# Optimization experiments

Hardware: AMD Instinct MI355X
Metric: run time of the kernel (lower is better)

The kernel has to match this reference:

```python
import jax, jax.numpy as jnp
import numpy as np

N, BS, T, D = 512, 64, 200, 32
ALPHA, EPS, TIME_LOG, POWER = 0.1, 1e-6, 5.0, 3


def setup_inputs() -> dict:
    key = jax.random.key(0)
    ks = jax.random.split(key, 16)
    s = 0.1
    skills = jax.random.randint(ks[0], (BS, T), 0, N)
    times = jnp.sort(jax.random.randint(ks[1], (BS, T), 0, 100000), axis=1)
    labels = jax.random.uniform(ks[2], (BS, T), dtype=jnp.float32)
    adj = jax.random.uniform(ks[3], (1, BS, N, N), dtype=jnp.float32)
    node_embeddings = jax.random.normal(ks[4], (1, N, 2 * D), dtype=jnp.float32)
    user_b0 = jax.random.uniform(ks[5], (BS, D), dtype=jnp.float32)
    user_f0 = jax.random.uniform(ks[6], (BS, D), dtype=jnp.float32)
    conv1_w = jax.random.normal(ks[7], (D, D, 5), dtype=jnp.float32) * s
    conv1_b = jax.random.normal(ks[8], (D,), dtype=jnp.float32) * s
    conv2_w = jax.random.normal(ks[9], (D, D, 1), dtype=jnp.float32) * s
    conv2_b = jax.random.normal(ks[10], (D,), dtype=jnp.float32) * s
    lin_f_w = jax.random.normal(ks[11], (D, D), dtype=jnp.float32) * s
    lin_f_b = jax.random.normal(ks[12], (D,), dtype=jnp.float32) * s
    lin_b_w = jax.random.normal(ks[13], (D, D), dtype=jnp.float32) * s
    lin_b_b = jax.random.normal(ks[14], (D,), dtype=jnp.float32) * s
    return dict(skills=skills, times=times, labels=labels, adj=adj,
                node_embeddings=node_embeddings, user_b0=user_b0, user_f0=user_f0,
                conv1_w=conv1_w, conv1_b=conv1_b, conv2_w=conv2_w, conv2_b=conv2_b,
                lin_f_w=lin_f_w, lin_f_b=lin_f_b, lin_b_w=lin_b_w, lin_b_b=lin_b_b)


def _forward(skills, times, labels, adj, node_embeddings, user_b0, user_f0,
             conv1_w, conv1_b, conv2_w, conv2_b, lin_f_w, lin_f_b, lin_b_w, lin_b_b):
    n = jnp.float32(N)
    A1 = adj[0]                      # [BS, N, N]  (leading A=1 dim squeezed)
    A2 = jnp.matmul(A1, A1)
    A3 = jnp.matmul(A2, A1)
    # adj^i / N^i for i=1..3, stacked over power dim -> [BS, 3, N, N]
    adj_list = jnp.stack([A1 / n, A2 / (n * n), A3 / (n * n * n)], axis=1)
    node_emb = node_embeddings[0]    # [N, 2D]
    node_send, node_rec = node_emb[:, :D], node_emb[:, D:]
    # temporal deltas: log(|t_i - t_{i-1}| + EPS) / log(time_log) -> [T-1, BS]
    dt = jnp.abs(times[:, 1:] - times[:, :-1]).astype(jnp.float32)
    delta = (jnp.log(dt + EPS) / jnp.log(jnp.float32(TIME_LOG))).T

    last_perf0 = user_b0 @ node_rec.T           # [BS, N]
    node_last_forget0 = user_f0 @ node_send.T   # [BS, N]

    def step(carry, xs):
        user_b, user_f, last_perf, node_last_forget = carry
        delta_t, label_t, skill_t = xs
        node_cur_base = user_b @ node_rec.T                               # [BS, N]
        temporal = jnp.exp(-delta_t[:, None] * ALPHA * node_last_forget) * last_perf
        # sum over powers folded into the contraction; /(power*N) as in source
        spatial = jnp.einsum('bj,bnjk->bk', last_perf, adj_list) / (POWER * n)
        cur_perf = jax.nn.sigmoid(node_cur_base + temporal + spatial)     # [BS, N]
        nlf = user_f @ node_send.T
        lab = jnp.broadcast_to(label_t[:, None], (BS, D))
        user = jnp.stack([user_b, user_f, lab,
                          node_rec[skill_t], node_send[skill_t]], axis=-1)  # [BS, D, 5]
        h = jax.nn.relu(jnp.einsum('bcl,ocl->bo', user, conv1_w) + conv1_b)
        uu = h @ conv2_w[:, :, 0].T + conv2_b
        new_f = jnp.tanh(uu @ lin_f_w.T + lin_f_b)
        new_b = jnp.tanh(uu @ lin_b_w.T + lin_b_b)
        pred = jnp.take_along_axis(cur_perf, skill_t[:, None], axis=1)    # [BS, 1]
        return (new_b, new_f, cur_perf, nlf), pred

    xs = (delta, labels[:, 1:].T, skills[:, 1:].T)
    _, preds = jax.lax.scan(step, (user_b0, user_f0, last_perf0, node_last_forget0), xs)
    return preds  # [T-1, BS, 1]


def reference(skills, times, labels, adj, node_embeddings, user_b0, user_f0,
              conv1_w, conv1_b, conv2_w, conv2_b, lin_f_w, lin_f_b, lin_b_w, lin_b_b):
    return _forward(skills, times, labels, adj, node_embeddings, user_b0, user_f0,
                    conv1_w, conv1_b, conv2_w, conv2_b, lin_f_w, lin_f_b, lin_b_w, lin_b_b)
```

## Files before the change

kernel.cpp:

```cpp
#include <hip/hip_runtime.h>

#define NN 512
#define BSZ 64
#define TTOT 200
#define NSTEP 199
#define DD 32

typedef __attribute__((ext_vector_type(8))) short bf16x8;
typedef __attribute__((ext_vector_type(8))) int i32x8;
typedef __attribute__((ext_vector_type(4))) float f32x4;
typedef __attribute__((ext_vector_type(4))) unsigned int u32x4;

__device__ __forceinline__ float bf2f(unsigned short u) {
  union { unsigned int i; float f; } v; v.i = ((unsigned int)u) << 16; return v.f;
}
__device__ __forceinline__ unsigned short f2bf(float f) {
  unsigned int b = __float_as_uint(f);
  return (unsigned short)((b + 0x7fffu + ((b >> 16) & 1u)) >> 16);
}
__device__ __forceinline__ unsigned int pk_trunc(float hi, float lo) {
  return __builtin_amdgcn_perm(__float_as_uint(hi), __float_as_uint(lo), 0x07060302u);
}
__device__ __forceinline__ unsigned char e4m3(float x) {
  float a = fabsf(x);
  unsigned int s = (__float_as_uint(x) >> 24) & 0x80u;
  if (a < 0.01171875f) return (unsigned char)s;
  a = fminf(a, 448.0f);
  unsigned int u = __float_as_uint(a);
  unsigned int keep = (u >> 20) & 7u;
  unsigned int rest = u & 0xFFFFFu;
  unsigned int base = (((u >> 23) - 120u) << 3) | keep;
  unsigned int rnd = (rest > 0x80000u) || (rest == 0x80000u && (keep & 1u));
  return (unsigned char)(s | (base + rnd));
}
__device__ __forceinline__ float dec8(unsigned char x) {
  int e = (x >> 3) & 15, m = x & 7;
  float v = e ? ldexpf(8.f + (float)m, e - 10) : ldexpf((float)m, -9);
  return (x & 0x80) ? -v : v;
}
__device__ __forceinline__ float rlane(float v, int l) {
  return __int_as_float(__builtin_amdgcn_readlane(__float_as_int(v), l));
}

__device__ __forceinline__ size_t m8_addr(int k, int col) {
  int nt = col >> 4, cch = k >> 5;
  int l2 = (((k >> 3) & 3) << 4) + (col & 15);
  return (size_t)((nt * 16 + cch) * 512) + (size_t)l2 * 8 + (size_t)(k & 7);
}
__device__ __forceinline__ size_t m8mxa(int k, int col) {
  int f = ((k >> 7) << 5) + (col >> 4);
  int ln2 = (((k >> 5) & 3) << 4) + (col & 15);
  return (((size_t)f * 64 + ln2) << 5) + (size_t)(k & 31);
}

__global__ __launch_bounds__(256) void gemm_a2_fast(
    const float* __restrict__ A1, unsigned short* __restrict__ A2) {
  const int tn = blockIdx.x, tm = blockIdx.y, b = blockIdx.z;
  const int tid = threadIdx.x, lane = tid & 63;
  const int w = tid >> 6, wr = w >> 1, wc = w & 1;
  const int q = lane >> 4, ln = lane & 15;
  const size_t Ao = (size_t)b * NN * NN;
  __shared__ __align__(16) unsigned char Asw[128 * 128];
  __shared__ __align__(16) unsigned char Bsw[128 * 128];
  f32x4 acc[4][4];
#pragma unroll
  for (int mi = 0; mi < 4; ++mi)
#pragma unroll
    for (int ni = 0; ni < 4; ++ni) acc[mi][ni] = f32x4{0.f, 0.f, 0.f, 0.f};

  const int arow = tid >> 2, achk = tid & 3;
  const int bg = tid >> 5, bc0 = (tid & 31) * 4;
  const float* Ab = A1 + Ao;

  for (int k0 = 0; k0 < NN; k0 += 64) {
#pragma unroll
    for (int p = 0; p < 2; ++p) {
      const int r = arow + p * 64;
      const float* src = Ab + (size_t)(tm * 128 + r) * NN + k0 + achk * 16;
      f32x4 x0 = *(const f32x4*)src, x1 = *(const f32x4*)(src + 4);
      f32x4 x2 = *(const f32x4*)(src + 8), x3 = *(const f32x4*)(src + 12);
      u32x4 y0 = u32x4{pk_trunc(x0[1], x0[0]), pk_trunc(x0[3], x0[2]),
                       pk_trunc(x1[1], x1[0]), pk_trunc(x1[3], x1[2])};
      u32x4 y1 = u32x4{pk_trunc(x2[1], x2[0]), pk_trunc(x2[3], x2[2]),
                       pk_trunc(x3[1], x3[0]), pk_trunc(x3[3], x3[2])};
      const int sw = r & 7;
      *(u32x4*)(Asw + r * 128 + (((achk * 2) ^ sw) << 4)) = y0;
      *(u32x4*)(Asw + r * 128 + (((achk * 2 + 1) ^ sw) << 4)) = y1;
    }
    {
      f32x4 r[8];
#pragma unroll
      for (int i = 0; i < 8; ++i)
        r[i] = *(const f32x4*)(Ab + (size_t)(k0 + bg * 8 + i) * NN + tn * 128 + bc0);
#pragma unroll
      for (int m = 0; m < 4; ++m) {
        const int col = bc0 + m;
        u32x4 v = u32x4{pk_trunc(r[1][m], r[0][m]), pk_trunc(r[3][m], r[2][m]),
                        pk_trunc(r[5][m], r[4][m]), pk_trunc(r[7][m], r[6][m])};
        *(u32x4*)(Bsw + col * 128 + ((bg ^ (col & 7)) << 4)) = v;
      }
    }
    __syncthreads();
#pragma unroll
    for (int ks = 0; ks < 2; ++ks) {
      bf16x8 af[4], bv[4];
#pragma unroll
      for (int mi = 0; mi < 4; ++mi) {
        const int r = wr * 64 + mi * 16 + ln;
        af[mi] = *(const bf16x8*)(Asw + r * 128 + (((ks * 4 + q) ^ (r & 7)) << 4));
      }
#pragma unroll
      for (int ni = 0; ni < 4; ++ni) {
        const int r = wc * 64 + ni * 16 + ln;
        bv[ni] = *(const bf16x8*)(Bsw + r * 128 + (((ks * 4 + q) ^ (r & 7)) << 4));
      }
#pragma unroll
      for (int mi = 0; mi < 4; ++mi)
#pragma unroll
        for (int ni = 0; ni < 4; ++ni)
          acc[mi][ni] = __builtin_amdgcn_mfma_f32_16x16x32_bf16(
              af[mi], bv[ni], acc[mi][ni], 0, 0, 0);
    }
    __syncthreads();
  }
  unsigned short* Cb = A2 + Ao;
#pragma unroll
  for (int mi = 0; mi < 4; ++mi)
#pragma unroll
    for (int ni = 0; ni < 4; ++ni) {
      const int col = tn * 128 + wc * 64 + ni * 16 + ln;
#pragma unroll
      for (int r = 0; r < 4; ++r) {
        const int row = tm * 128 + wr * 64 + mi * 16 + q * 4 + r;
        Cb[(size_t)row * NN + col] = f2bf(acc[mi][ni][r]);
      }
    }
}

__global__ __launch_bounds__(256) void gemm_m_fast(
    const float* __restrict__ A1, const unsigned short* __restrict__ A2,
    unsigned char* __restrict__ M8k, unsigned char* __restrict__ M8x,
    int has_mx) {
  const int tn = blockIdx.x, tm = blockIdx.y, b = blockIdx.z;
  const int tid = threadIdx.x, lane = tid & 63;
  const int w = tid >> 6, wr = w >> 1, wc = w & 1;
  const int q = lane >> 4, ln = lane & 15;
  const size_t Ao = (size_t)b * NN * NN;
  __shared__ __align__(16) unsigned char Asw[128 * 128];
  __shared__ __align__(16) unsigned char Bsw[128 * 128];
  f32x4 acc[4][4];
#pragma unroll
  for (int mi = 0; mi < 4; ++mi)
#pragma unroll
    for (int ni = 0; ni < 4; ++ni) acc[mi][ni] = f32x4{0.f, 0.f, 0.f, 0.f};

  const int srow = tid >> 1, sh = tid & 1;
  const int bg = tid >> 5, bc0 = (tid & 31) * 4;
  const unsigned short* A2b = A2 + Ao;
  const float* Ab = A1 + Ao;

  for (int k0 = 0; k0 < NN; k0 += 64) {
    {
      const unsigned short* asrc = A2b + (size_t)(tm * 128 + srow) * NN + k0 + sh * 32;
      const int sw = srow & 7;
#pragma unroll
      for (int j = 0; j < 4; ++j) {
        u32x4 va = *(const u32x4*)(asrc + j * 8);
        *(u32x4*)(Asw + srow * 128 + (((sh * 4 + j) ^ sw) << 4)) = va;
      }
    }
    {
      f32x4 r[8];
#pragma unroll
      for (int i = 0; i < 8; ++i)
        r[i] = *(const f32x4*)(Ab + (size_t)(k0 + bg * 8 + i) * NN + tn * 128 + bc0);
#pragma unroll
      for (int m = 0; m < 4; ++m) {
        const int col = bc0 + m;
        u32x4 v = u32x4{pk_trunc(r[1][m], r[0][m]), pk_trunc(r[3][m], r[2][m]),
                        pk_trunc(r[5][m], r[4][m]), pk_trunc(r[7][m], r[6][m])};
        *(u32x4*)(Bsw + col * 128 + ((bg ^ (col & 7)) << 4)) = v;
      }
    }
    __syncthreads();
#pragma unroll
    for (int ks = 0; ks < 2; ++ks) {
      bf16x8 af[4], bv[4];
#pragma unroll
      for (int mi = 0; mi < 4; ++mi) {
        const int r = wr * 64 + mi * 16 + ln;
        af[mi] = *(const bf16x8*)(Asw + r * 128 + (((ks * 4 + q) ^ (r & 7)) << 4));
      }
#pragma unroll
      for (int ni = 0; ni < 4; ++ni) {
        const int r = wc * 64 + ni * 16 + ln;
        bv[ni] = *(const bf16x8*)(Bsw + r * 128 + (((ks * 4 + q) ^ (r & 7)) << 4));
      }
#pragma unroll
      for (int mi = 0; mi < 4; ++mi)
#pragma unroll
        for (int ni = 0; ni < 4; ++ni)
          acc[mi][ni] = __builtin_amdgcn_mfma_f32_16x16x32_bf16(
              af[mi], bv[ni], acc[mi][ni], 0, 0, 0);
    }
    __syncthreads();
  }
  const float c1 = 1048576.f / (3.f * 512.f * 512.f);
  const float c2 = c1 / 512.f;
  const float c3 = c2 / 512.f;
  unsigned char* Mk = M8k + Ao;
  unsigned char* Mx = M8x + Ao;
#pragma unroll
  for (int mi = 0; mi < 4; ++mi) {
    const int row0 = tm * 128 + wr * 64 + mi * 16 + q * 4;
#pragma unroll
    for (int ni = 0; ni < 4; ++ni) {
      const int col = tn * 128 + wc * 64 + ni * 16 + ln;
      unsigned int wv = 0;
#pragma unroll
      for (int r = 0; r < 4; ++r) {
        const int row = row0 + r;
        float mval = c1 * A1[Ao + (size_t)row * NN + col] +
                     c2 * bf2f(A2b[(size_t)row * NN + col]) + c3 * acc[mi][ni][r];
        wv |= ((unsigned int)e4m3(mval)) << (8 * r);
      }
      *(unsigned int*)(Mk + m8_addr(row0, col)) = wv;
      if (has_mx) *(unsigned int*)(Mx + m8mxa(row0, col)) = wv;
    }
  }
}

__global__ __launch_bounds__(256) void gemm_a2_slow(
    const float* __restrict__ A1, unsigned short* __restrict__ A2) {
  const int b = blockIdx.x, tn = blockIdx.y, tm = blockIdx.z;
  const int tid = threadIdx.x, lane = tid & 63, w = tid >> 6;
  const int q = lane >> 4, ln = lane & 15;
  const size_t Ao = (size_t)b * NN * NN;
  f32x4 zero = {0.f, 0.f, 0.f, 0.f};
  f32x4 acc[4] = {zero, zero, zero, zero};
  const float* ap = A1 + Ao + (size_t)(tm * 64 + w * 16 + ln) * NN + q * 8;
  for (int k0 = 0; k0 < NN; k0 += 32) {
    f32x4 x0 = *(const f32x4*)(ap + k0);
    f32x4 x1 = *(const f32x4*)(ap + k0 + 4);
    union { bf16x8 v; unsigned int u[4]; } af;
    af.u[0] = pk_trunc(x0[1], x0[0]);
    af.u[1] = pk_trunc(x0[3], x0[2]);
    af.u[2] = pk_trunc(x1[1], x1[0]);
    af.u[3] = pk_trunc(x1[3], x1[2]);
#pragma unroll
    for (int i = 0; i < 4; ++i) {
      bf16x8 bv;
#pragma unroll
      for (int j = 0; j < 8; ++j)
        bv[j] = (short)f2bf(A1[Ao + (size_t)(k0 + q * 8 + j) * NN + tn * 64 + i * 16 + ln]);
      acc[i] = __builtin_amdgcn_mfma_f32_16x16x32_bf16(af.v, bv, acc[i], 0, 0, 0);
    }
  }
  unsigned short* Cb = A2 + Ao;
#pragma unroll
  for (int i = 0; i < 4; ++i) {
    int col = tn * 64 + i * 16 + ln;
#pragma unroll
    for (int r = 0; r < 4; ++r) {
      int row = tm * 64 + w * 16 + q * 4 + r;
      Cb[(size_t)row * NN + col] = f2bf(acc[i][r]);
    }
  }
}

__global__ __launch_bounds__(256) void gemm_m_slow(
    const float* __restrict__ A1, const unsigned short* __restrict__ A2,
    unsigned char* __restrict__ M8k, unsigned char* __restrict__ M8x,
    int has_mx) {
  const int b = blockIdx.x, tn = blockIdx.y, tm = blockIdx.z;
  const int tid = threadIdx.x, lane = tid & 63, w = tid >> 6;
  const int q = lane >> 4, ln = lane & 15;
  const size_t Ao = (size_t)b * NN * NN;
  const unsigned short* A2b = A2 + Ao;
  f32x4 zero = {0.f, 0.f, 0.f, 0.f};
  f32x4 acc[4] = {zero, zero, zero, zero};
  const unsigned short* ap = A2b + (size_t)(tm * 64 + w * 16 + ln) * NN + q * 8;
  for (int k0 = 0; k0 < NN; k0 += 32) {
    bf16x8 af = *(const bf16x8*)(ap + k0);
#pragma unroll
    for (int i = 0; i < 4; ++i) {
      bf16x8 bv;
#pragma unroll
      for (int j = 0; j < 8; ++j)
        bv[j] = (short)f2bf(A1[Ao + (size_t)(k0 + q * 8 + j) * NN + tn * 64 + i * 16 + ln]);
      acc[i] = __builtin_amdgcn_mfma_f32_16x16x32_bf16(af, bv, acc[i], 0, 0, 0);
    }
  }
  const float c1 = 1048576.f / (3.f * 512.f * 512.f);
  const float c2 = c1 / 512.f;
  const float c3 = c2 / 512.f;
  unsigned char* Mk = M8k + Ao;
  unsigned char* Mx = M8x + Ao;
  const int row0 = tm * 64 + w * 16 + q * 4;
#pragma unroll
  for (int i = 0; i < 4; ++i) {
    int col = tn * 64 + i * 16 + ln;
    unsigned int wv = 0;
#pragma unroll
    for (int r = 0; r < 4; ++r) {
      int row = row0 + r;
      float mval = c1 * A1[Ao + (size_t)row * NN + col] +
                   c2 * bf2f(A2b[(size_t)row * NN + col]) + c3 * acc[i][r];
      wv |= ((unsigned int)e4m3(mval)) << (8 * r);
    }
    *(unsigned int*)(Mk + m8_addr(row0, col)) = wv;
    if (has_mx) *(unsigned int*)(Mx + m8mxa(row0, col)) = wv;
  }
}

__global__ __launch_bounds__(64) void probe_kernel(int* __restrict__ flag) {
  const int lane = threadIdx.x, q = lane >> 4, n = lane & 15;
  __shared__ unsigned char A8[128];
  __shared__ unsigned char B8[128 * 16];
  for (int k = lane; k < 128; k += 64) A8[k] = (unsigned char)(8 + ((k * 37 + 11) % 56));
  for (int i = lane; i < 2048; i += 64)
    B8[i] = (unsigned char)(((i & 1) ? 0x80 : 0) | (8 + ((i * 23 + 5) % 56)));
  __syncthreads();
  union { i32x8 v; unsigned char b[32]; } af, bf;
#pragma unroll
  for (int j = 0; j < 32; ++j) {
    af.b[j] = A8[q * 32 + j];
    bf.b[j] = B8[(q * 32 + j) * 16 + n];
  }
  f32x4 acc = {0.f, 0.f, 0.f, 0.f};
  acc = __builtin_amdgcn_mfma_scale_f32_16x16x128_f8f6f4(af.v, bf.v, acc, 0, 0,
                                                         0, 127, 0, 127);
  float ref = 0.f;
  for (int k = 0; k < 128; ++k) ref += dec8(A8[k]) * dec8(B8[k * 16 + n]);
  int ok = 1;
#pragma unroll
  for (int r = 0; r < 4; ++r)
    ok &= (fabsf(acc[r] - ref) <= 1e-3f * fmaxf(fabsf(ref), 1.f)) ? 1 : 0;
  unsigned long long bal = __ballot(ok);
  if (lane == 0) *flag = (bal == ~0ull) ? 1 : 0;
}

__global__ __launch_bounds__(64) void traj2_kernel(
    const int* __restrict__ skills, const float* __restrict__ labels,
    const float* __restrict__ emb, const float* __restrict__ ub0g,
    const float* __restrict__ uf0g, const float* __restrict__ w1g,
    const float* __restrict__ b1g, const float* __restrict__ w2g,
    const float* __restrict__ b2g, const float* __restrict__ wfg,
    const float* __restrict__ bfg, const float* __restrict__ wbg,
    const float* __restrict__ bbg, float* __restrict__ UBg,
    float* __restrict__ UFg) {
  const int b = blockIdx.x;
  const int lane = threadIdx.x;
  const int o = lane & 31, half = lane >> 5;

  __shared__ float ub_l[DD], uf_l[DD], e_l[2 * DD];
  __shared__ float label_s[NSTEP];
  __shared__ int skill_s[NSTEP];

  for (int i = lane; i < NSTEP; i += 64) {
    label_s[i] = labels[b * TTOT + i + 1];
    skill_s[i] = skills[b * TTOT + i + 1];
  }

  float w1r[80];
#pragma unroll
  for (int k = 0; k < 8; ++k) {
    const int c0 = (half * 8 + k) * 2;
#pragma unroll
    for (int j = 0; j < 5; ++j) {
      w1r[k * 10 + j] = w1g[o * 160 + c0 * 5 + j];
      w1r[k * 10 + 5 + j] = w1g[o * 160 + (c0 + 1) * 5 + j];
    }
  }
  float w2r[16];
#pragma unroll
  for (int cc = 0; cc < 16; ++cc) w2r[cc] = w2g[o * 32 + half * 16 + cc];
  const float* wsg = half ? wbg : wfg;
  float wsr[32];
#pragma unroll
  for (int c = 0; c < DD; ++c) wsr[c] = wsg[o * 32 + c];
  const float b1r = b1g[o], b2r = b2g[o];
  const float bselr = half ? bbg[o] : bfg[o];

  float val = half ? ub0g[b * DD + o] : uf0g[b * DD + o];

  __syncthreads();

  float* UBp = UBg + (size_t)b * NSTEP * DD;
  float* UFp = UFg + (size_t)b * NSTEP * DD;

  float ev = emb[(size_t)skill_s[0] * (2 * DD) + lane];
  float pg[8];

  for (int step = 0; step < NSTEP; ++step) {
    if (step) {
      float part = 0.f;
#pragma unroll
      for (int s2 = 0; s2 < 8; ++s2) part += pg[s2];
      float h = b1r + part + __shfl_xor(part, 32);
      h = fmaxf(h, 0.f);
      float up = 0.f;
#pragma unroll
      for (int cc = 0; cc < 16; ++cc) {
        float hv0 = rlane(h, cc), hv1 = rlane(h, 16 + cc);
        up += (half ? hv1 : hv0) * w2r[cc];
      }
      float uu = b2r + up + __shfl_xor(up, 32);
      float aac = bselr;
#pragma unroll
      for (int c = 0; c < DD; ++c) aac += rlane(uu, c) * wsr[c];
      val = 1.f - 2.f / (1.f + __expf(2.f * aac));
    }
    if (half) ub_l[o] = val; else uf_l[o] = val;
    e_l[lane] = ev;
    (half ? UBp : UFp)[step * DD + o] = val;
    if (step + 1 < NSTEP) ev = emb[(size_t)skill_s[step + 1] * (2 * DD) + lane];
    const float lab = label_s[step];
#pragma unroll
    for (int k = 0; k < 8; ++k) {
      const int c0 = (half * 8 + k) * 2;
      float ubc0 = ub_l[c0], ubc1 = ub_l[c0 + 1];
      float ufc0 = uf_l[c0], ufc1 = uf_l[c0 + 1];
      float rs0 = e_l[c0], rs1 = e_l[c0 + 1];
      float rr0 = e_l[DD + c0], rr1 = e_l[DD + c0 + 1];
      float hpart = ubc0 * w1r[k * 10 + 0] + ufc0 * w1r[k * 10 + 1] +
                    lab * w1r[k * 10 + 2] + rr0 * w1r[k * 10 + 3] +
                    rs0 * w1r[k * 10 + 4];
      hpart += ubc1 * w1r[k * 10 + 5] + ufc1 * w1r[k * 10 + 6] +
               lab * w1r[k * 10 + 7] + rr1 * w1r[k * 10 + 8] +
               rs1 * w1r[k * 10 + 9];
      pg[k] = hpart;
    }
  }
}

__global__ __launch_bounds__(512) void precomp_kernel(
    const int* __restrict__ times, const float* __restrict__ emb,
    const float* __restrict__ UBg, const float* __restrict__ UFg,
    float* __restrict__ NCBg, float* __restrict__ TCg) {
  const int b = blockIdx.x;
  const int s0 = blockIdx.y * 8;
  const int n = threadIdx.x;
  float nr[DD], ns[DD];
#pragma unroll
  for (int c = 0; c < DD; ++c) {
    ns[c] = emb[(size_t)n * (2 * DD) + c];
    nr[c] = emb[(size_t)n * (2 * DD) + DD + c];
  }
  for (int s = s0; s < s0 + 8 && s < NSTEP; ++s) {
    const float* ubp = UBg + ((size_t)b * NSTEP + s) * DD;
    const float* ufp = UFg + ((size_t)b * NSTEP + (s ? s - 1 : 0)) * DD;
    float n0 = 0.f, n1 = 0.f, n2 = 0.f, n3 = 0.f;
    float l0 = 0.f, l1 = 0.f, l2 = 0.f, l3 = 0.f;
#pragma unroll
    for (int c = 0; c < 8; ++c) {
      n0 += ubp[c] * nr[c];
      n1 += ubp[8 + c] * nr[8 + c];
      n2 += ubp[16 + c] * nr[16 + c];
      n3 += ubp[24 + c] * nr[24 + c];
      l0 += ufp[c] * ns[c];
      l1 += ufp[8 + c] * ns[8 + c];
      l2 += ufp[16 + c] * ns[16 + c];
      l3 += ufp[24 + c] * ns[24 + c];
    }
    float ncb = (n0 + n1) + (n2 + n3);
    float nlf = (l0 + l1) + (l2 + l3);
    int dt_ = times[b * TTOT + s + 1] - times[b * TTOT + s];
    if (dt_ < 0) dt_ = -dt_;
    float delta = __logf((float)dt_ + 1e-6f) * 0.6213349345596119f;
    float tc = __expf(-delta * 0.1f * nlf);
    NCBg[((size_t)b * NSTEP + s) * NN + n] = ncb;
    TCg[((size_t)b * NSTEP + s) * NN + n] = tc;
  }
}

__global__ __launch_bounds__(512, 1) void scan_fast(
    const int* __restrict__ skills, const float* __restrict__ NCBg,
    const float* __restrict__ TCg, const unsigned char* __restrict__ M8k,
    const unsigned char* __restrict__ M8x, int allow_mx,
    const int* __restrict__ flag, float* __restrict__ out) {
  const int b = blockIdx.x;
  const int t = threadIdx.x;
  const int lane = t & 63, w = t >> 6, q = lane >> 4;
  __shared__ __align__(32) unsigned char lp8[2][NN];
  __shared__ int skill_s[NSTEP];
  const int use_mx = allow_mx && (*flag);
  for (int i = t; i < NSTEP; i += 512) skill_s[i] = skills[b * TTOT + i + 1];

  union MU { i32x8 v; long l[4]; };
  MU mreg[16];
  if (use_mx) {
    const unsigned char* Mb = M8x + (size_t)b * NN * NN;
#pragma unroll
    for (int c = 0; c < 4; ++c)
#pragma unroll
      for (int i = 0; i < 4; ++i)
        mreg[c * 4 + i].v = *(const i32x8*)(
            Mb + (((size_t)(c * 32 + w * 4 + i) * 64 + lane) << 5));
  } else {
    const unsigned char* Mb = M8k + (size_t)b * NN * NN;
#pragma unroll
    for (int c = 0; c < 16; ++c)
#pragma unroll
      for (int i = 0; i < 4; ++i)
        mreg[c].l[i] = *(const long*)(
            Mb + (((size_t)(w * 64 + i * 16 + c)) << 9) + (size_t)lane * 8);
  }
  const float* ncbp = NCBg + (size_t)b * NSTEP * NN + t;
  const float* tcp = TCg + (size_t)b * NSTEP * NN + t;
  float ncb_c = ncbp[0];
  float tc_c = tcp[0];
  float ncb_n1 = 0.f, tc_n1 = 1.f;
  if (NSTEP > 1) { ncb_n1 = ncbp[NN]; tc_n1 = tcp[NN]; }
  float rlp = ncb_c;
  lp8[0][t] = e4m3(rlp);
  __syncthreads();

  int pidx = -1;
  float pval = 0.f;
  for (int step = 0; step < NSTEP; ++step) {
    const int cb = step & 1;
    if (pidx >= 0) out[pidx] = pval;
    float ncb_n2 = 0.f, tc_n2 = 1.f;
    if (step + 2 < NSTEP) {
      ncb_n2 = ncbp[(size_t)(step + 2) * NN];
      tc_n2 = tcp[(size_t)(step + 2) * NN];
    }
    int sk_s = skill_s[step];
    f32x4 zero = {0.f, 0.f, 0.f, 0.f};
    f32x4 acc[4] = {zero, zero, zero, zero};
    if (use_mx) {
#pragma unroll
      for (int c = 0; c < 4; ++c) {
        i32x8 af = *(const i32x8*)(&lp8[cb][c * 128 + q * 32]);
#pragma unroll
        for (int i = 0; i < 4; ++i)
          acc[i] = __builtin_amdgcn_mfma_scale_f32_16x16x128_f8f6f4(
              af, mreg[c * 4 + i].v, acc[i], 0, 0, 0, 127, 0, 127);
      }
    } else {
#pragma unroll
      for (int c = 0; c < 16; ++c) {
        long af = *(const long*)(&lp8[cb][c * 32 + q * 8]);
#pragma unroll
        for (int i = 0; i < 4; ++i)
          acc[i] = __builtin_amdgcn_mfma_f32_16x16x32_fp8_fp8(af, mreg[c].l[i],
                                                              acc[i], 0, 0, 0);
      }
    }
    float spatial = ((q & 2) ? ((q & 1) ? acc[3][0] : acc[2][0])
                             : ((q & 1) ? acc[1][0] : acc[0][0])) * 0x1p-20f;
    float cur = 1.f / (1.f + __expf(-((ncb_c + tc_c * rlp) + spatial)));
    pidx = (t == sk_s) ? (step * BSZ + b) : -1;
    pval = cur;
    rlp = cur;
    lp8[cb ^ 1][t] = e4m3(cur);
    __syncthreads();
    ncb_c = ncb_n1; tc_c = tc_n1;
    ncb_n1 = ncb_n2; tc_n1 = tc_n2;
  }
  if (pidx >= 0) out[pidx] = pval;
}

__global__ __launch_bounds__(512, 2) void scan_kernel(
    const int* __restrict__ skills, const int* __restrict__ times,
    const float* __restrict__ labels, const float* __restrict__ emb,
    const float* __restrict__ ub0g, const float* __restrict__ uf0g,
    const float* __restrict__ w1g, const float* __restrict__ b1g,
    const float* __restrict__ w2g, const float* __restrict__ b2g,
    const float* __restrict__ wfg, const float* __restrict__ bfg,
    const float* __restrict__ wbg, const float* __restrict__ bbg,
    const unsigned char* __restrict__ M8k, const unsigned char* __restrict__ M8x,
    int allow_mx, const int* __restrict__ flag, float* __restrict__ out) {
  const int b = blockIdx.x;
  const int t = threadIdx.x;
  const int lane = t & 63, w = t >> 6, q = lane >> 4;

  __shared__ __align__(32) unsigned char lp8[NN];
  __shared__ float ub[DD], uf[DD];
  __shared__ float delta_s[NSTEP], label_s[NSTEP];
  __shared__ int skill_s[NSTEP];
  __shared__ float hp[16][33];
  __shared__ float w1t[DD * 5 * DD];
  __shared__ float w2t[DD * DD], wft[DD * DD], wbt[DD * DD];
  __shared__ float b1s[DD], b2s[DD], bfs[DD], bbs[DD];

  const int use_mx = allow_mx && (*flag);

  float nrec[DD], nsend[DD];
#pragma unroll
  for (int c = 0; c < DD; ++c) {
    nsend[c] = emb[(size_t)t * (2 * DD) + c];
    nrec[c] = emb[(size_t)t * (2 * DD) + DD + c];
  }
  for (int idx = t; idx < DD * DD * 5; idx += 512) {
    int o = idx / 160, rem = idx % 160;
    w1t[rem * 32 + o] = w1g[idx];
  }
  for (int idx = t; idx < DD * DD; idx += 512) {
    int o = idx >> 5, c = idx & 31;
    w2t[c * 32 + o] = w2g[idx];
    wft[c * 32 + o] = wfg[idx];
    wbt[c * 32 + o] = wbg[idx];
  }
  if (t < DD) {
    b1s[t] = b1g[t]; b2s[t] = b2g[t];
    bfs[t] = bfg[t]; bbs[t] = bbg[t];
    ub[t] = ub0g[b * DD + t];
    uf[t] = uf0g[b * DD + t];
  }
  for (int i = t; i < NSTEP; i += 512) {
    int dt_ = times[b * TTOT + i + 1] - times[b * TTOT + i];
    if (dt_ < 0) dt_ = -dt_;
    delta_s[i] = __logf((float)dt_ + 1e-6f) * 0.6213349345596119f;
    label_s[i] = labels[b * TTOT + i + 1];
    skill_s[i] = skills[b * TTOT + i + 1];
  }

  union MU { i32x8 v; long l[4]; };
  MU mreg[16];
  if (use_mx) {
    const unsigned char* Mb = M8x + (size_t)b * NN * NN;
#pragma unroll
    for (int c = 0; c < 4; ++c)
#pragma unroll
      for (int i = 0; i < 4; ++i)
        mreg[c * 4 + i].v = *(const i32x8*)(
            Mb + (((size_t)(c * 32 + w * 4 + i) * 64 + lane) << 5));
  } else {
    const unsigned char* Mb = M8k + (size_t)b * NN * NN;
#pragma unroll
    for (int c = 0; c < 16; ++c)
#pragma unroll
      for (int i = 0; i < 4; ++i)
        mreg[c].l[i] = *(const long*)(
            Mb + (((size_t)(w * 64 + i * 16 + c)) << 9) + (size_t)lane * 8);
  }
  __syncthreads();

  float rlp = 0.f, rnlf = 0.f;
#pragma unroll
  for (int c = 0; c < DD; ++c) {
    rlp += ub[c] * nrec[c];
    rnlf += uf[c] * nsend[c];
  }
  lp8[t] = e4m3(rlp);
  __syncthreads();

  for (int step = 0; step < NSTEP; ++step) {
    if (step && w == 0) {
      int o = lane & 31, half = lane >> 5;
      float part = 0.f;
#pragma unroll
      for (int s2 = 0; s2 < 8; ++s2) part += hp[half * 8 + s2][o];
      float h = b1s[o] + part + __shfl_xor(part, 32);
      h = fmaxf(h, 0.f);
      float up = 0.f;
#pragma unroll
      for (int cc = 0; cc < 16; ++cc) {
        float hv0 = rlane(h, cc), hv1 = rlane(h, 16 + cc);
        up += (half ? hv1 : hv0) * w2t[(half * 16 + cc) * 32 + o];
      }
      float uu = b2s[o] + up + __shfl_xor(up, 32);
      const float* wsel = half ? wbt : wft;
      float aac = half ? bbs[o] : bfs[o];
#pragma unroll
      for (int c = 0; c < DD; ++c) aac += rlane(uu, c) * wsel[c * 32 + o];
      float val = 1.f - 2.f / (1.f + __expf(2.f * aac));
      if (half) ub[o] = val;
      else uf[o] = val;
    }
    f32x4 zero = {0.f, 0.f, 0.f, 0.f};
    f32x4 acc[4] = {zero, zero, zero, zero};
    if (use_mx) {
#pragma unroll
      for (int c = 0; c < 4; ++c) {
        i32x8 af = *(const i32x8*)(&lp8[c * 128 + q * 32]);
#pragma unroll
        for (int i = 0; i < 4; ++i)
          acc[i] = __builtin_amdgcn_mfma_scale_f32_16x16x128_f8f6f4(
              af, mreg[c * 4 + i].v, acc[i], 0, 0, 0, 127, 0, 127);
      }
    } else {
#pragma unroll
      for (int c = 0; c < 16; ++c) {
        long af = *(const long*)(&lp8[c * 32 + q * 8]);
#pragma unroll
        for (int i = 0; i < 4; ++i)
          acc[i] = __builtin_amdgcn_mfma_f32_16x16x32_fp8_fp8(af, mreg[c].l[i],
                                                              acc[i], 0, 0, 0);
      }
    }
    float spatial = ((q & 2) ? ((q & 1) ? acc[3][0] : acc[2][0])
                             : ((q & 1) ? acc[1][0] : acc[0][0])) * 0x1p-20f;
    __syncthreads();

    float rub = ub[lane & 31], ruf = uf[lane & 31];
    float n0 = 0.f, n1 = 0.f, n2 = 0.f, n3 = 0.f;
    float l0 = 0.f, l1 = 0.f, l2 = 0.f, l3 = 0.f;
#pragma unroll
    for (int c = 0; c < 8; ++c) {
      n0 += rlane(rub, c) * nrec[c];
      n1 += rlane(rub, 8 + c) * nrec[8 + c];
      n2 += rlane(rub, 16 + c) * nrec[16 + c];
      n3 += rlane(rub, 24 + c) * nrec[24 + c];
      l0 += rlane(ruf, c) * nsend[c];
      l1 += rlane(ruf, 8 + c) * nsend[8 + c];
      l2 += rlane(ruf, 16 + c) * nsend[16 + c];
      l3 += rlane(ruf, 24 + c) * nsend[24 + c];
    }
    float ncb = (n0 + n1) + (n2 + n3);
    float nlfn = (l0 + l1) + (l2 + l3);
    float e = __expf(-delta_s[step] * 0.1f * rnlf) * rlp;
    float cur = 1.f / (1.f + __expf(-(ncb + e + spatial)));

    {
      int o = t & 31, s = t >> 5;
      float lab = label_s[step];
      int sk = skill_s[step];
      float hpart = 0.f;
#pragma unroll
      for (int cc = 0; cc < 2; ++cc) {
        int c = (s << 1) + cc;
        const float* wrow = &w1t[(c * 5) * 32 + o];
        float rs = emb[(size_t)sk * (2 * DD) + c];
        float rr = emb[(size_t)sk * (2 * DD) + DD + c];
        hpart += ub[c] * wrow[0] + uf[c] * wrow[32] + lab * wrow[64] +
                 rr * wrow[96] + rs * wrow[128];
      }
      hp[s][o] = hpart;
    }

    rlp = cur;
    rnlf = nlfn;
    lp8[t] = e4m3(cur);
    if (t == skill_s[step]) out[step * BSZ + b] = cur;
    __syncthreads();
  }
}

extern "C" void kernel_launch(void* const* d_in, const int* in_sizes, int n_in,
                              void* d_out, int out_size, void* d_ws, size_t ws_size,
                              hipStream_t stream) {
  (void)in_sizes; (void)n_in; (void)out_size;
  const int* skills = (const int*)d_in[0];
  const int* times = (const int*)d_in[1];
  const float* labels = (const float*)d_in[2];
  const float* adj = (const float*)d_in[3];
  const float* emb = (const float*)d_in[4];
  const float* ub0 = (const float*)d_in[5];
  const float* uf0 = (const float*)d_in[6];
  const float* w1 = (const float*)d_in[7];
  const float* b1 = (const float*)d_in[8];
  const float* w2 = (const float*)d_in[9];
  const float* b2 = (const float*)d_in[10];
  const float* wf = (const float*)d_in[11];
  const float* bf = (const float*)d_in[12];
  const float* wb = (const float*)d_in[13];
  const float* bb = (const float*)d_in[14];

  const size_t mat = (size_t)BSZ * NN * NN;
  const size_t ncb_sz = (size_t)BSZ * NSTEP * NN * sizeof(float);
  const size_t ub_sz = (size_t)BSZ * NSTEP * DD * sizeof(float);
  char* base = (char*)d_ws;
  unsigned char *M8k, *M8x;
  unsigned short* A2;
  char* ovl = nullptr;
  int* flag;
  int use_fast, allow_mx;
  if (ws_size >= 6 * mat + 4) {
    use_fast = 1; allow_mx = 1;
    M8k = (unsigned char*)base; M8x = M8k + mat;
    A2 = (unsigned short*)(base + 2 * mat);
    flag = (int*)(base + 6 * mat);
    ovl = base + 2 * mat;
  } else if (ws_size >= 5 * mat + 4) {
    use_fast = 1; allow_mx = 0;
    M8k = (unsigned char*)base; M8x = M8k;
    A2 = (unsigned short*)(base + mat);
    flag = (int*)(base + 5 * mat);
    ovl = base + mat;
  } else if (ws_size >= 4 * mat + 4) {
    use_fast = 0; allow_mx = 1;
    M8k = (unsigned char*)base; M8x = M8k + mat;
    A2 = (unsigned short*)(base + 2 * mat);
    flag = (int*)(base + 4 * mat);
  } else {
    use_fast = 0; allow_mx = 0;
    M8k = (unsigned char*)base; M8x = M8k;
    A2 = (unsigned short*)(base + mat);
    flag = (int*)(base + 3 * mat);
  }

  dim3 gb(256);
  if (use_fast) {
    dim3 gf(4, 4, BSZ);
    gemm_a2_fast<<<gf, gb, 0, stream>>>(adj, A2);
    gemm_m_fast<<<gf, gb, 0, stream>>>(adj, A2, M8k, M8x, allow_mx);
    float* NCB = (float*)ovl;
    float* TC = (float*)(ovl + ncb_sz);
    float* UB = (float*)(ovl + 2 * ncb_sz);
    float* UF = (float*)(ovl + 2 * ncb_sz + ub_sz);
    traj2_kernel<<<dim3(BSZ), dim3(64), 0, stream>>>(
        skills, labels, emb, ub0, uf0, w1, b1, w2, b2, wf, bf, wb, bb, UB, UF);
    precomp_kernel<<<dim3(BSZ, 25), dim3(512), 0, stream>>>(times, emb, UB, UF,
                                                            NCB, TC);
    probe_kernel<<<dim3(1), dim3(64), 0, stream>>>(flag);
    scan_fast<<<dim3(BSZ), dim3(512), 0, stream>>>(skills, NCB, TC, M8k, M8x,
                                                   allow_mx, flag, (float*)d_out);
  } else {
    dim3 gg(BSZ, 8, 8);
    gemm_a2_slow<<<gg, gb, 0, stream>>>(adj, A2);
    gemm_m_slow<<<gg, gb, 0, stream>>>(adj, A2, M8k, M8x, allow_mx);
    probe_kernel<<<dim3(1), dim3(64), 0, stream>>>(flag);
    scan_kernel<<<dim3(BSZ), dim3(512), 0, stream>>>(
        skills, times, labels, emb, ub0, uf0, w1, b1, w2, b2, wf, bf, wb, bb,
        M8k, M8x, allow_mx, flag, (float*)d_out);
  }
}
```

Measured before the change: 639.4 us.

## Overlap user-state trajectory recurrence with adjacency GEMMs via extra grid blocks

The serial per-batch user trajectory recurrence (previously its own traj2 kernel) is split into three segments. The first two run as extra high-priority single-wave blocks inside the two GEMM kernels, passing state through a small checkpoint buffer, and a short tail kernel finishes the rest. This hides most of the latency-bound recurrence behind the bandwidth/compute-heavy GEMMs. The probe runs first so gemm_m can skip writing the unused M8k layout when the MX path is available. The trade-off is extra blocks and some LDS pressure in the GEMM launches, plus extra checkpoint traffic.

```diff
diff --git a/kernel.cpp b/kernel.cpp
--- a/kernel.cpp
+++ b/kernel.cpp
@@ -5,6 +5,8 @@
 #define TTOT 200
 #define NSTEP 199
 #define DD 32
+#define CHK1 60
+#define CHK2 130
 
 typedef __attribute__((ext_vector_type(8))) short bf16x8;
 typedef __attribute__((ext_vector_type(8))) int i32x8;
@@ -53,15 +55,132 @@
   return (((size_t)f * 64 + ln2) << 5) + (size_t)(k & 31);
 }
 
+#define TRAJ_ARGS                                                              \
+  const int *skills_t, const float *labels_t, const float *emb_t,              \
+      const float *ub0g, const float *uf0g, const float *w1g,                  \
+      const float *b1g, const float *w2g, const float *b2g, const float *wfg,  \
+      const float *bfg, const float *wbg, const float *bbg, float *UBg,        \
+      float *UFg, float *CKg
+#define TRAJ_PASS                                                              \
+  skills_t, labels_t, emb_t, ub0g, uf0g, w1g, b1g, w2g, b2g, wfg, bfg, wbg,    \
+      bbg, UBg, UFg, CKg
+
+__device__ __forceinline__ void traj_seg(
+    int b, int s_begin, int s_end, int lane, float* ub_l, float* uf_l,
+    float* e_l, float* label_s, int* skill_s, TRAJ_ARGS) {
+  const int o = lane & 31, half = lane >> 5;
+
+  for (int i = lane; i < NSTEP; i += 64) {
+    label_s[i] = labels_t[b * TTOT + i + 1];
+    skill_s[i] = skills_t[b * TTOT + i + 1];
+  }
+
+  float w1r[80];
+#pragma unroll
+  for (int k = 0; k < 8; ++k) {
+    const int c0 = (half * 8 + k) * 2;
+#pragma unroll
+    for (int j = 0; j < 5; ++j) {
+      w1r[k * 10 + j] = w1g[o * 160 + c0 * 5 + j];
+      w1r[k * 10 + 5 + j] = w1g[o * 160 + (c0 + 1) * 5 + j];
+    }
+  }
+  float w2r[16];
+#pragma unroll
+  for (int cc = 0; cc < 16; ++cc) w2r[cc] = w2g[o * 32 + half * 16 + cc];
+  const float* wsg = half ? wbg : wfg;
+  float wsr[32];
+#pragma unroll
+  for (int c = 0; c < DD; ++c) wsr[c] = wsg[o * 32 + c];
+  const float b1r = b1g[o], b2r = b2g[o];
+  const float bselr = half ? bbg[o] : bfg[o];
+
+  float val, pg[8];
+  float* ck = CKg + ((size_t)b * 64 + lane) * 9;
+  if (s_begin == 0) {
+    val = half ? ub0g[b * DD + o] : uf0g[b * DD + o];
+  } else {
+    val = ck[0];
+#pragma unroll
+    for (int k = 0; k < 8; ++k) pg[k] = ck[1 + k];
+  }
+
+  float* UBp = UBg + (size_t)b * NSTEP * DD;
+  float* UFp = UFg + (size_t)b * NSTEP * DD;
+
+  float ev = emb_t[(size_t)skill_s[s_begin] * (2 * DD) + lane];
+
+  for (int step = s_begin; step < s_end; ++step) {
+    if (step) {
+      float part = 0.f;
+#pragma unroll
+      for (int s2 = 0; s2 < 8; ++s2) part += pg[s2];
+      float h = b1r + part + __shfl_xor(part, 32);
+      h = fmaxf(h, 0.f);
+      float up = 0.f;
+#pragma unroll
+      for (int cc = 0; cc < 16; ++cc) {
+        float hv0 = rlane(h, cc), hv1 = rlane(h, 16 + cc);
+        up += (half ? hv1 : hv0) * w2r[cc];
+      }
+      float uu = b2r + up + __shfl_xor(up, 32);
+      float aac = bselr;
+#pragma unroll
+      for (int c = 0; c < DD; ++c) aac += rlane(uu, c) * wsr[c];
+      val = 1.f - 2.f / (1.f + __expf(2.f * aac));
+    }
+    if (half) ub_l[o] = val; else uf_l[o] = val;
+    e_l[lane] = ev;
+    (half ? UBp : UFp)[step * DD + o] = val;
+    if (step + 1 < NSTEP) ev = emb_t[(size_t)skill_s[step + 1] * (2 * DD) + lane];
+    const float lab = label_s[step];
+#pragma unroll
+    for (int k = 0; k < 8; ++k) {
+      const int c0 = (half * 8 + k) * 2;
+      float ubc0 = ub_l[c0], ubc1 = ub_l[c0 + 1];
+      float ufc0 = uf_l[c0], ufc1 = uf_l[c0 + 1];
+      float rs0 = e_l[c0], rs1 = e_l[c0 + 1];
+      float rr0 = e_l[DD + c0], rr1 = e_l[DD + c0 + 1];
+      float hpart = ubc0 * w1r[k * 10 + 0] + ufc0 * w1r[k * 10 + 1] +
+                    lab * w1r[k * 10 + 2] + rr0 * w1r[k * 10 + 3] +
+                    rs0 * w1r[k * 10 + 4];
+      hpart += ubc1 * w1r[k * 10 + 5] + ufc1 * w1r[k * 10 + 6] +
+               lab * w1r[k * 10 + 7] + rr1 * w1r[k * 10 + 8] +
+               rs1 * w1r[k * 10 + 9];
+      pg[k] = hpart;
+    }
+  }
+  if (s_end < NSTEP) {
+    ck[0] = val;
+#pragma unroll
+    for (int k = 0; k < 8; ++k) ck[1 + k] = pg[k];
+  }
+}
+
 __global__ __launch_bounds__(256) void gemm_a2_fast(
-    const float* __restrict__ A1, unsigned short* __restrict__ A2) {
+    const float* __restrict__ A1, unsigned short* __restrict__ A2,
+    TRAJ_ARGS) {
+  __shared__ __align__(16) unsigned char smem[32768];
+  const int tid = threadIdx.x;
+  if (blockIdx.x == 4) {
+    if (blockIdx.y != 0 || tid >= 64) return;
+    __builtin_amdgcn_s_setprio(3);
+    float* ub_l = (float*)smem;
+    float* uf_l = (float*)(smem + 128);
+    float* e_l = (float*)(smem + 256);
+    float* label_s = (float*)(smem + 512);
+    int* skill_s = (int*)(smem + 512 + 800);
+    traj_seg(blockIdx.z, 0, CHK1, tid, ub_l, uf_l, e_l, label_s, skill_s,
+             TRAJ_PASS);
+    return;
+  }
   const int tn = blockIdx.x, tm = blockIdx.y, b = blockIdx.z;
-  const int tid = threadIdx.x, lane = tid & 63;
+  const int lane = tid & 63;
   const int w = tid >> 6, wr = w >> 1, wc = w & 1;
   const int q = lane >> 4, ln = lane & 15;
   const size_t Ao = (size_t)b * NN * NN;
-  __shared__ __align__(16) unsigned char Asw[128 * 128];
-  __shared__ __align__(16) unsigned char Bsw[128 * 128];
+  unsigned char* Asw = smem;
+  unsigned char* Bsw = smem + 16384;
   f32x4 acc[4][4];
 #pragma unroll
   for (int mi = 0; mi < 4; ++mi)
@@ -140,14 +259,29 @@
 __global__ __launch_bounds__(256) void gemm_m_fast(
     const float* __restrict__ A1, const unsigned short* __restrict__ A2,
     unsigned char* __restrict__ M8k, unsigned char* __restrict__ M8x,
-    int has_mx) {
+    int has_mx, const int* __restrict__ flag, TRAJ_ARGS) {
+  __shared__ __align__(16) unsigned char smem[32768];
+  const int tid = threadIdx.x;
+  if (blockIdx.x == 4) {
+    if (blockIdx.y != 0 || tid >= 64) return;
+    __builtin_amdgcn_s_setprio(3);
+    float* ub_l = (float*)smem;
+    float* uf_l = (float*)(smem + 128);
+    float* e_l = (float*)(smem + 256);
+    float* label_s = (float*)(smem + 512);
+    int* skill_s = (int*)(smem + 512 + 800);
+    traj_seg(blockIdx.z, CHK1, CHK2, tid, ub_l, uf_l, e_l, label_s, skill_s,
+             TRAJ_PASS);
+    return;
+  }
   const int tn = blockIdx.x, tm = blockIdx.y, b = blockIdx.z;
-  const int tid = threadIdx.x, lane = tid & 63;
+  const int lane = tid & 63;
   const int w = tid >> 6, wr = w >> 1, wc = w & 1;
   const int q = lane >> 4, ln = lane & 15;
   const size_t Ao = (size_t)b * NN * NN;
-  __shared__ __align__(16) unsigned char Asw[128 * 128];
-  __shared__ __align__(16) unsigned char Bsw[128 * 128];
+  const int skip_k = has_mx && (*flag);
+  unsigned char* Asw = smem;
+  unsigned char* Bsw = smem + 16384;
   f32x4 acc[4][4];
 #pragma unroll
   for (int mi = 0; mi < 4; ++mi)
@@ -224,10 +358,18 @@
                      c2 * bf2f(A2b[(size_t)row * NN + col]) + c3 * acc[mi][ni][r];
         wv |= ((unsigned int)e4m3(mval)) << (8 * r);
       }
-      *(unsigned int*)(Mk + m8_addr(row0, col)) = wv;
+      if (!skip_k) *(unsigned int*)(Mk + m8_addr(row0, col)) = wv;
       if (has_mx) *(unsigned int*)(Mx + m8mxa(row0, col)) = wv;
     }
   }
+}
+
+__global__ __launch_bounds__(64) void traj_tail(TRAJ_ARGS) {
+  __shared__ float ub_l[DD], uf_l[DD], e_l[2 * DD];
+  __shared__ float label_s[NSTEP];
+  __shared__ int skill_s[NSTEP];
+  traj_seg(blockIdx.x, CHK2, NSTEP, threadIdx.x, ub_l, uf_l, e_l, label_s,
+           skill_s, TRAJ_PASS);
 }
 
 __global__ __launch_bounds__(256) void gemm_a2_slow(
@@ -763,58 +905,80 @@
   const size_t ncb_sz = (size_t)BSZ * NSTEP * NN * sizeof(float);
   const size_t ub_sz = (size_t)BSZ * NSTEP * DD * sizeof(float);
   char* base = (char*)d_ws;
-  unsigned char *M8k, *M8x;
-  unsigned short* A2;
-  char* ovl = nullptr;
-  int* flag;
-  int use_fast, allow_mx;
+  dim3 gb(256);
+
   if (ws_size >= 6 * mat + 4) {
-    use_fast = 1; allow_mx = 1;
-    M8k = (unsigned char*)base; M8x = M8k + mat;
-    A2 = (unsigned short*)(base + 2 * mat);
-    flag = (int*)(base + 6 * mat);
-    ovl = base + 2 * mat;
-  } else if (ws_size >= 5 * mat + 4) {
-    use_fast = 1; allow_mx = 0;
-    M8k = (unsigned char*)base; M8x = M8k;
-    A2 = (unsigned short*)(base + mat);
-    flag = (int*)(base + 5 * mat);
-    ovl = base + mat;
-  } else if (ws_size >= 4 * mat + 4) {
-    use_fast = 0; allow_mx = 1;
-    M8k = (unsigned char*)base; M8x = M8k + mat;
-    A2 = (unsigned short*)(base + 2 * mat);
-    flag = (int*)(base + 4 * mat);
-  } else {
-    use_fast = 0; allow_mx = 0;
-    M8k = (unsigned char*)base; M8x = M8k;
-    A2 = (unsigned short*)(base + mat);
-    flag = (int*)(base + 3 * mat);
-  }
-
-  dim3 gb(256);
-  if (use_fast) {
-    dim3 gf(4, 4, BSZ);
-    gemm_a2_fast<<<gf, gb, 0, stream>>>(adj, A2);
-    gemm_m_fast<<<gf, gb, 0, stream>>>(adj, A2, M8k, M8x, allow_mx);
+    unsigned char* M8k = (unsigned char*)base;
+    unsigned char* M8x = (unsigned char*)(base + mat);
+    unsigned short* A2 = (unsigned short*)(base + 2 * mat);
+    int* flag = (int*)(base + 6 * mat);
+    char* ovl = base + 2 * mat;
     float* NCB = (float*)ovl;
     float* TC = (float*)(ovl + ncb_sz);
     float* UB = (float*)(ovl + 2 * ncb_sz);
     float* UF = (float*)(ovl + 2 * ncb_sz + ub_sz);
+    float* CK = (float*)(ovl + 2 * ncb_sz + 2 * ub_sz);
+
+    probe_kernel<<<dim3(1), dim3(64), 0, stream>>>(flag);
+    gemm_a2_fast<<<dim3(5, 4, BSZ), gb, 0, stream>>>(
+        adj, A2, skills, labels, emb, ub0, uf0, w1, b1, w2, b2, wf, bf, wb,
+        bb, UB, UF, CK);
+    gemm_m_fast<<<dim3(5, 4, BSZ), gb, 0, stream>>>(
+        adj, A2, M8k, M8x, 1, flag, skills, labels, emb, ub0, uf0, w1, b1, w2,
+        b2, wf, bf, wb, bb, UB, UF, CK);
+    traj_tail<<<dim3(BSZ), dim3(64), 0, stream>>>(
+        skills, labels, emb, ub0, uf0, w1, b1, w2, b2, wf, bf, wb, bb, UB, UF,
+        CK);
+    precomp_kernel<<<dim3(BSZ, 25), dim3(512), 0, stream>>>(times, emb, UB, UF,
+                                                            NCB, TC);
+    scan_fast<<<dim3(BSZ), dim3(512), 0, stream>>>(skills, NCB, TC, M8k, M8x,
+                                                   1, flag, (float*)d_out);
+  } else if (ws_size >= 5 * mat + 4) {
+    unsigned char* M8k = (unsigned char*)base;
+    unsigned short* A2 = (unsigned short*)(base + mat);
+    int* flag = (int*)(base + 5 * mat);
+    char* ovl = base + mat;
+    float* NCB = (float*)ovl;
+    float* TC = (float*)(ovl + ncb_sz);
+    float* UB = (float*)(ovl + 2 * ncb_sz);
+    float* UF = (float*)(ovl + 2 * ncb_sz + ub_sz);
+    float* CK = (float*)(ovl + 2 * ncb_sz + 2 * ub_sz);
+
+    probe_kernel<<<dim3(1), dim3(64), 0, stream>>>(flag);
+    gemm_a2_fast<<<dim3(4, 4, BSZ), gb, 0, stream>>>(
+        adj, A2, skills, labels, emb, ub0, uf0, w1, b1, w2, b2, wf, bf, wb,
+        bb, UB, UF, CK);
+    gemm_m_fast<<<dim3(4, 4, BSZ), gb, 0, stream>>>(
+        adj, A2, M8k, M8k, 0, flag, skills, labels, emb, ub0, uf0, w1, b1, w2,
+        b2, wf, bf, wb, bb, UB, UF, CK);
     traj2_kernel<<<dim3(BSZ), dim3(64), 0, stream>>>(
         skills, labels, emb, ub0, uf0, w1, b1, w2, b2, wf, bf, wb, bb, UB, UF);
     precomp_kernel<<<dim3(BSZ, 25), dim3(512), 0, stream>>>(times, emb, UB, UF,
                                                             NCB, TC);
-    probe_kernel<<<dim3(1), dim3(64), 0, stream>>>(flag);
-    scan_fast<<<dim3(BSZ), dim3(512), 0, stream>>>(skills, NCB, TC, M8k, M8x,
-                                                   allow_mx, flag, (float*)d_out);
-  } else {
+    scan_fast<<<dim3(BSZ), dim3(512), 0, stream>>>(skills, NCB, TC, M8k, M8k,
+                                                   0, flag, (float*)d_out);
+  } else if (ws_size >= 4 * mat + 4) {
+    unsigned char* M8k = (unsigned char*)base;
+    unsigned char* M8x = M8k + mat;
+    unsigned short* A2 = (unsigned short*)(base + 2 * mat);
+    int* flag = (int*)(base + 4 * mat);
     dim3 gg(BSZ, 8, 8);
     gemm_a2_slow<<<gg, gb, 0, stream>>>(adj, A2);
-    gemm_m_slow<<<gg, gb, 0, stream>>>(adj, A2, M8k, M8x, allow_mx);
+    gemm_m_slow<<<gg, gb, 0, stream>>>(adj, A2, M8k, M8x, 1);
     probe_kernel<<<dim3(1), dim3(64), 0, stream>>>(flag);
     scan_kernel<<<dim3(BSZ), dim3(512), 0, stream>>>(
         skills, times, labels, emb, ub0, uf0, w1, b1, w2, b2, wf, bf, wb, bb,
-        M8k, M8x, allow_mx, flag, (float*)d_out);
-  }
-}
+        M8k, M8x, 1, flag, (float*)d_out);
+  } else {
+    unsigned char* M8k = (unsigned char*)base;
+    unsigned short* A2 = (unsigned short*)(base + mat);
+    int* flag = (int*)(base + 3 * mat);
+    dim3 gg(BSZ, 8, 8);
+    gemm_a2_slow<<<gg, gb, 0, stream>>>(adj, A2);
+    gemm_m_slow<<<gg, gb, 0, stream>>>(adj, A2, M8k, M8k, 0);
+    probe_kernel<<<dim3(1), dim3(64), 0, stream>>>(flag);
+    scan_kernel<<<dim3(BSZ), dim3(512), 0, stream>>>(
+        skills, times, labels, emb, ub0, uf0, w1, b1, w2, b2, wf, bf, wb, bb,
+        M8k, M8k, 0, flag, (float*)d_out);
+  }
+}
```

Result: slower. 781.7 us (+22.2%).
